# Kernel optimization log

Hardware: AMD Instinct MI355X
Metric: run time of the kernel (lower is better)

The kernel has to match this reference:

```python
import jax, jax.numpy as jnp
import numpy as np

NUM_CLASSES = 21
THRESH = 0.5
NEG_POS = 3
VAR0, VAR1 = 0.1, 0.2


def point_form(boxes):
    # center form (cx,cy,w,h) -> corner form (x1,y1,x2,y2)
    return jnp.concatenate([boxes[:, :2] - boxes[:, 2:] / 2,
                            boxes[:, :2] + boxes[:, 2:] / 2], axis=1)


def jaccard(a, b):
    # a: [N,4] corner form, b: [P,4] corner form -> IoU [N,P]
    lt = jnp.maximum(a[:, None, :2], b[None, :, :2])
    rb = jnp.minimum(a[:, None, 2:], b[None, :, 2:])
    wh = jnp.clip(rb - lt, 0.0)
    inter = wh[..., 0] * wh[..., 1]
    area_a = (a[:, 2] - a[:, 0]) * (a[:, 3] - a[:, 1])
    area_b = (b[:, 2] - b[:, 0]) * (b[:, 3] - b[:, 1])
    return inter / (area_a[:, None] + area_b[None, :] - inter)


def match_one(truths, labels, priors):
    # truths: [N,4] corner form, labels: [N] int, priors: [P,4] center form
    ov = jaccard(truths, point_form(priors))            # [N,P]
    best_prior_idx = jnp.argmax(ov, axis=1)             # [N] best prior per truth
    best_truth_ov = jnp.max(ov, axis=0)                 # [P]
    best_truth_idx = jnp.argmax(ov, axis=0)             # [P]
    # ensure each truth keeps its best prior
    best_truth_ov = best_truth_ov.at[best_prior_idx].set(2.0)
    best_truth_idx = best_truth_idx.at[best_prior_idx].set(
        jnp.arange(truths.shape[0], dtype=best_truth_idx.dtype))
    matches = truths[best_truth_idx]                    # [P,4]
    conf = labels[best_truth_idx] + 1                   # [P]
    conf = jnp.where(best_truth_ov < THRESH, 0, conf)
    # encode
    g_cxcy = ((matches[:, :2] + matches[:, 2:]) / 2 - priors[:, :2]) / (VAR0 * priors[:, 2:])
    g_wh = jnp.log((matches[:, 2:] - matches[:, :2]) / priors[:, 2:]) / VAR1
    return jnp.concatenate([g_cxcy, g_wh], axis=1), conf


def setup_inputs() -> dict:
    key = jax.random.key(0)
    k1, k2, k3, k4, k5, k6, k7 = jax.random.split(key, 7)
    B, P, C, N = 64, 24564, NUM_CLASSES, 16
    loc_data = jax.random.normal(k1, (B, P, 4), dtype=jnp.float32)
    conf_data = jax.random.normal(k2, (B, P, C), dtype=jnp.float32)
    # priors: valid center-form boxes
    ctr = 0.05 + 0.9 * jax.random.uniform(k3, (P, 2), dtype=jnp.float32)
    pwh = 0.05 + 0.25 * jax.random.uniform(k4, (P, 2), dtype=jnp.float32)
    priors = jnp.concatenate([ctr, pwh], axis=1)
    # truths: valid corner-form boxes
    xy1 = 0.7 * jax.random.uniform(k5, (B, N, 2), dtype=jnp.float32)
    twh = 0.05 + 0.2 * jax.random.uniform(k6, (B, N, 2), dtype=jnp.float32)
    truths = jnp.concatenate([xy1, xy1 + twh], axis=2)
    labels = jax.random.randint(k7, (B, N), 0, 20, dtype=jnp.int32)
    return {"loc_data": loc_data, "conf_data": conf_data, "priors": priors,
            "truths": truths, "labels": labels}


def reference(loc_data, conf_data, priors, truths, labels):
    B, P, C = conf_data.shape
    loc_t, conf_t = jax.vmap(lambda t, l: match_one(t, l, priors))(truths, labels)
    pos = conf_t > 0                                     # [B,P]

    # localization smooth-L1, summed over positives
    diff = loc_data - loc_t
    ad = jnp.abs(diff)
    sl1 = jnp.where(ad < 1.0, 0.5 * diff * diff, ad - 0.5)
    loss_l = jnp.sum(sl1 * pos[..., None].astype(loc_data.dtype))

    # per-prior CE = logsumexp - logit at matched class
    lse = jax.nn.logsumexp(conf_data, axis=2)            # [B,P]
    gathered = jnp.take_along_axis(conf_data, conf_t[..., None].astype(jnp.int32), axis=2)[..., 0]
    loss_c_all = lse - gathered

    # hard-negative mining via double argsort rank (pos zeroed first)
    loss_c_mine = jnp.where(pos, 0.0, loss_c_all)
    idx_rank = jnp.argsort(jnp.argsort(-loss_c_mine, axis=1), axis=1)
    num_pos = jnp.sum(pos, axis=1, keepdims=True)        # [B,1]
    num_neg = jnp.minimum(NEG_POS * num_pos, P - 1)
    neg = idx_rank < num_neg

    mask = pos | neg
    loss_c = jnp.sum(jnp.where(mask, loss_c_all, 0.0))

    n = jnp.sum(num_pos).astype(loc_data.dtype)
    return loss_l / n, loss_c / n
```

## Files before the change

### kernel.cpp

```cpp
#include <hip/hip_runtime.h>
#include <cstdint>
#include <cstddef>

#define B_ 64
#define P_ 24564
#define C_ 21
#define N_ 16
#define NPL_ 96
#define THRESH_ 0.5f


__device__ inline unsigned long long shfl_down_u64(unsigned long long v, int off) {
    unsigned lo = (unsigned)v, hi = (unsigned)(v >> 32);
    lo = __shfl_down(lo, off);
    hi = __shfl_down(hi, off);
    return ((unsigned long long)hi << 32) | lo;
}

__device__ inline void async_copy16(const float* g, float* l) {
    __builtin_amdgcn_global_load_lds(
        (const __attribute__((address_space(1))) void*)g,
        (__attribute__((address_space(3))) void*)l, 16, 0, 0);
}

__device__ inline float sl1_encode(float4 ld, float4 pr,
                                   float tx1, float ty1, float tx2, float ty2) {
    float gcx = ((tx1 + tx2) * 0.5f - pr.x) / (0.1f * pr.z);
    float gcy = ((ty1 + ty2) * 0.5f - pr.y) / (0.1f * pr.w);
    float gw  = __logf((tx2 - tx1) / pr.z) / 0.2f;
    float gh  = __logf((ty2 - ty1) / pr.w) / 0.2f;
    float g[4] = {gcx, gcy, gw, gh};
    float l[4] = {ld.x, ld.y, ld.z, ld.w};
    float s = 0.0f;
#pragma unroll
    for (int i = 0; i < 4; i++) {
        float d = l[i] - g[i];
        float ad = fabsf(d);
        s += (ad < 1.0f) ? 0.5f * d * d : ad - 0.5f;
    }
    return s;
}

__device__ inline void scan_hist(const int* h, int M, int kk,
                                 int* outB, int* outR) {
    int lane = threadIdx.x & 63;
    int CH = M >> 6;
    int base = M - (lane + 1) * CH;
    int s = 0;
    for (int j = 0; j < CH; j++) s += h[base + j];
    int incl = s;
#pragma unroll
    for (int off = 1; off < 64; off <<= 1) {
        int v = __shfl_up(incl, off);
        if (lane >= off) incl += v;
    }
    int excl = incl - s;
    if (excl < kk && excl + s >= kk) {
        int acc = excl;
        for (int bin = base + CH - 1; bin >= base; bin--) {
            int c = h[bin];
            if (acc + c >= kk) { *outB = bin; *outR = kk - acc; break; }
            acc += c;
        }
    }
}


__global__ __launch_bounds__(256) void
kF_fused(const float* __restrict__ loc,
         const float* __restrict__ conf,
         const float* __restrict__ priors,
         const float* __restrict__ truths,
         const int* __restrict__ labels,
         float* __restrict__ mine,
         float* __restrict__ part_ll,
         float* __restrict__ part_pce,
         int* __restrict__ part_np,
         unsigned long long* __restrict__ part_key) {
    int b = blockIdx.y, bx = blockIdx.x, t = threadIdx.x;
    int wid = t >> 6, lane = t & 63;
    __shared__ float scf[4 * 1536];
    __shared__ float sll[4], spc[4];
    __shared__ int snp[4];
    unsigned* skey = (unsigned*)scf;

    int base_p = bx * 256;
    int nvalid = min(256, P_ - base_p);
    int maxf4 = (nvalid * C_) >> 2;
    const float* gtile = conf + ((size_t)b * P_ + base_p) * C_;

    int p0 = base_p + t;
    bool valid = t < nvalid;
    float4 pr = ((const float4*)priors)[valid ? p0 : base_p];
    float px1 = pr.x - pr.z * 0.5f, py1 = pr.y - pr.w * 0.5f;
    float px2 = pr.x + pr.z * 0.5f, py2 = pr.y + pr.w * 0.5f;
    float ap = (px2 - px1) * (py2 - py1);

    float* slice = scf + wid * 1536;
    int wf4 = wid * 336;
#pragma unroll
    for (int i = 0; i < 6; i++) {
        int f4 = wf4 + i * 64 + lane;
        int s4 = (f4 < maxf4) ? f4 : (maxf4 - 1);
        async_copy16(gtile + (size_t)s4 * 4, slice + i * 256);
    }

    unsigned u[N_];
    float best = -1.0f;
    int bn = 0;
#pragma unroll
    for (int n = 0; n < N_; n++) {
        float4 tb = ((const float4*)truths)[b * N_ + n];
        float at = (tb.z - tb.x) * (tb.w - tb.y);
        float lx = fmaxf(tb.x, px1), ly = fmaxf(tb.y, py1);
        float rx = fminf(tb.z, px2), ry = fminf(tb.w, py2);
        float w = fmaxf(rx - lx, 0.0f), h = fmaxf(ry - ly, 0.0f);
        float inter = w * h;
        float iou = inter / (at + ap - inter);
        if (iou > best) { best = iou; bn = n; }
        u[n] = valid ? __float_as_uint(iou) : 0u;
    }
    int pos = (valid && best >= THRESH_) ? 1 : 0;
    int bl = labels[b * N_ + bn];

    asm volatile("s_waitcnt vmcnt(0)" ::: "memory");

    float ll = 0.0f, pce = 0.0f;
    int np = 0;
    if (valid) {
        int cls = pos ? (bl + 1) : 0;
        const float* row = scf + wid * 1536 + lane * 21;
        float ssum = 0.0f;
#pragma unroll
        for (int i = 0; i < 21; i++) ssum += __expf(row[i]);
        float g = row[cls];
        float lca = fmaxf(__logf(ssum) - g, 0.0f);

        mine[(size_t)b * P_ + p0] = pos ? 0.0f : lca;

        if (pos) {
            np = 1;
            pce = lca;
            float4 ld = ((const float4*)loc)[(size_t)b * P_ + p0];
            float4 tb = ((const float4*)truths)[b * N_ + bn];
            ll = sl1_encode(ld, pr, tb.x, tb.y, tb.z, tb.w);
        }
    }

    for (int off = 32; off; off >>= 1) {
        ll += __shfl_down(ll, off);
        pce += __shfl_down(pce, off);
        np += __shfl_down(np, off);
    }
    if (lane == 0) { sll[wid] = ll; spc[wid] = pce; snp[wid] = np; }

    __syncthreads();
#pragma unroll
    for (int n = 0; n < N_; n++) skey[n * 256 + t] = u[n];
    __syncthreads();

#pragma unroll
    for (int i = 0; i < 4; i++) {
        int n = wid + 4 * i;
        unsigned long long bk = 0ull;
#pragma unroll
        for (int q = 0; q < 4; q++) {
            int tt = lane + 64 * q;
            unsigned k32 = skey[n * 256 + tt];
            unsigned long long v = ((unsigned long long)k32 << 32) |
                                   (unsigned)~(unsigned)tt;
            bk = (v > bk) ? v : bk;
        }
        for (int off = 32; off; off >>= 1) {
            unsigned long long o = shfl_down_u64(bk, off);
            bk = (o > bk) ? o : bk;
        }
        if (lane == 0) {
            int twin = (int)~(unsigned)(bk & 0xFFFFFFFFull);
            int pwin = base_p + twin;
            part_key[(size_t)(b * NPL_ + bx) * N_ + n] =
                (bk & 0xFFFFFFFF00000000ull) | (unsigned)~(unsigned)pwin;
        }
    }
    if (t == 0) {
        float a = 0.0f, cc = 0.0f;
        int q = 0;
        for (int i = 0; i < 4; i++) { a += sll[i]; cc += spc[i]; q += snp[i]; }
        part_ll[b * NPL_ + bx] = a;
        part_pce[b * NPL_ + bx] = cc;
        part_np[b * NPL_ + bx] = q;
    }
}

__global__ __launch_bounds__(1024) void
kB_batch(const float* __restrict__ loc,
         const float* __restrict__ conf,
         const float* __restrict__ priors,
         const float* __restrict__ truths,
         const int* __restrict__ labels,
         const float* __restrict__ mine,
         const float* __restrict__ part_ll,
         const float* __restrict__ part_pce,
         const int* __restrict__ part_np,
         const unsigned long long* __restrict__ part_key,
         double* __restrict__ bll,
         double* __restrict__ bpc,
         int* __restrict__ bnp) {
    int b = blockIdx.x, t = threadIdx.x, wid = t >> 6, lane = t & 63;
    __shared__ float tr[N_ * 4];
    __shared__ int lb[N_];
    __shared__ unsigned long long skmax[N_];
    __shared__ int sp[N_];
    __shared__ float sdll, sdpce, sll_s, spc_s;
    __shared__ int sdnp, snp_s;
    __shared__ int hist[4 * 2048];
    __shared__ int hist2[1024];
    __shared__ int hist3[1024];
    __shared__ int sB[3], sR[3];
    __shared__ float wsum[16];
    __shared__ int wcgt[16];

    if (t < N_ * 4) tr[t] = truths[b * N_ * 4 + t];
    if (t < N_) { lb[t] = labels[b * N_ + t]; skmax[t] = 0ull; }
#pragma unroll
    for (int i = 0; i < 8; i++) hist[t + (i << 10)] = 0;
    hist2[t] = 0;
    hist3[t] = 0;
    if (t == 0) { sdll = 0.f; sdpce = 0.f; sdnp = 0; sll_s = 0.f; spc_s = 0.f; snp_s = 0; }
    __syncthreads();
    if (t < 256) {
        int n = t & 15, j = t >> 4;
        unsigned long long bk = 0ull;
        for (int i = j; i < NPL_; i += 16) {
            unsigned long long k = part_key[(size_t)(b * NPL_ + i) * N_ + n];
            bk = (k > bk) ? k : bk;
        }
        atomicMax(&skmax[n], bk);
    }
    if (t < 128) {
        float a = 0.f, c2 = 0.f;
        int q = 0;
        if (t < NPL_) {
            a = part_ll[b * NPL_ + t];
            c2 = part_pce[b * NPL_ + t];
            q = part_np[b * NPL_ + t];
        }
        for (int off = 32; off; off >>= 1) {
            a += __shfl_down(a, off);
            c2 += __shfl_down(c2, off);
            q += __shfl_down(q, off);
        }
        if (lane == 0) {
            atomicAdd(&sll_s, a);
            atomicAdd(&spc_s, c2);
            atomicAdd(&snp_s, q);
        }
    }
    __syncthreads();
    if (t < N_) sp[t] = (int)~(unsigned)(skmax[t] & 0xFFFFFFFFull);
    __syncthreads();
    if (t < N_) {
        int p = sp[t];
        bool last = true;
        for (int n = t + 1; n < N_; n++) if (sp[n] == p) last = false;
        if (last) {
            int nf = t;
            float4 pr = ((const float4*)priors)[p];
            float px1 = pr.x - pr.z * 0.5f, py1 = pr.y - pr.w * 0.5f;
            float px2 = pr.x + pr.z * 0.5f, py2 = pr.y + pr.w * 0.5f;
            float ap = (px2 - px1) * (py2 - py1);
            float best = -1.0f;
            int bti = 0;
            for (int n = 0; n < N_; n++) {
                float tx1 = tr[n * 4], ty1 = tr[n * 4 + 1];
                float tx2 = tr[n * 4 + 2], ty2 = tr[n * 4 + 3];
                float at = (tx2 - tx1) * (ty2 - ty1);
                float lx = fmaxf(tx1, px1), ly = fmaxf(ty1, py1);
                float rx = fminf(tx2, px2), ry = fminf(ty2, py2);
                float w = fmaxf(rx - lx, 0.0f), h = fmaxf(ry - ly, 0.0f);
                float inter = w * h;
                float iou = inter / (at + ap - inter);
                if (iou > best) { best = iou; bti = n; }
            }
            int pos_old = (best >= THRESH_) ? 1 : 0;
            const float* cp = conf + ((size_t)b * P_ + p) * C_;
            float ssum = 0.0f;
            for (int j = 0; j < C_; j++) ssum += __expf(cp[j]);
            float lse = __logf(ssum);
            float4 ld = ((const float4*)loc)[(size_t)b * P_ + p];
            float dll = sl1_encode(ld, pr, tr[nf * 4], tr[nf * 4 + 1],
                                   tr[nf * 4 + 2], tr[nf * 4 + 3]);
            float dpce = lse - cp[lb[nf] + 1];
            int dnp = 1 - pos_old;
            if (pos_old) {
                dll -= sl1_encode(ld, pr, tr[bti * 4], tr[bti * 4 + 1],
                                  tr[bti * 4 + 2], tr[bti * 4 + 3]);
                dpce -= lse - cp[lb[bti] + 1];
            }
            atomicAdd(&sdll, dll);
            atomicAdd(&sdpce, dpce);
            atomicAdd(&sdnp, dnp);
        }
    }

    unsigned omask = 0;
#pragma unroll
    for (int n = 0; n < N_; n++) {
        int p = sp[n];
        if ((p & 1023) == t) omask |= 1u << (p >> 10);
    }
    const float* v = mine + (size_t)b * P_;
    int nel = (t < (P_ - 23 * 1024)) ? 24 : 23;
    float xv[24];
#pragma unroll
    for (int i = 0; i < 24; i++) {
        float x = 0.0f;
        if (i < nel) x = v[t + (i << 10)];
        if ((omask >> i) & 1) x = 0.0f;
        xv[i] = x;
    }

    int rep = (wid & 3) << 11;
#pragma unroll
    for (int i = 0; i < 24; i++) {
        if (i < nel) {
            unsigned bb = __float_as_uint(xv[i]);
            atomicAdd(&hist[rep + (bb >> 20)], 1);
        }
    }
    __syncthreads();
    {
        int h0 = hist[t] + hist[t + 2048] + hist[t + 4096] + hist[t + 6144];
        int h1 = hist[t + 1024] + hist[t + 3072] + hist[t + 5120] + hist[t + 7168];
        hist[t] = h0;
        hist[t + 1024] = h1;
    }
    __syncthreads();

    int np = snp_s + sdnp;
    int k = np * 3;
    if (k > P_ - 1) k = P_ - 1;

    unsigned T = 0x7FFFFFFFu;
    if (k > 0) {
        if (wid == 0) scan_hist(hist, 2048, k, &sB[0], &sR[0]);
        __syncthreads();
        unsigned B1 = (unsigned)sB[0];
        int k1 = sR[0];
#pragma unroll
        for (int i = 0; i < 24; i++) {
            if (i < nel) {
                unsigned bb = __float_as_uint(xv[i]);
                if ((bb >> 20) == B1) atomicAdd(&hist2[(bb >> 10) & 0x3FF], 1);
            }
        }
        __syncthreads();
        if (wid == 0) scan_hist(hist2, 1024, k1, &sB[1], &sR[1]);
        __syncthreads();
        unsigned hi = (B1 << 10) | (unsigned)sB[1];
        int k2 = sR[1];
#pragma unroll
        for (int i = 0; i < 24; i++) {
            if (i < nel) {
                unsigned bb = __float_as_uint(xv[i]);
                if ((bb >> 10) == hi) atomicAdd(&hist3[bb & 0x3FF], 1);
            }
        }
        __syncthreads();
        if (wid == 0) scan_hist(hist3, 1024, k2, &sB[2], &sR[2]);
        __syncthreads();
        T = (hi << 10) | (unsigned)sB[2];
    }

    float psum = 0.0f;
    int cgt = 0;
#pragma unroll
    for (int i = 0; i < 24; i++) {
        if (__float_as_uint(xv[i]) > T) { psum += xv[i]; cgt++; }
    }
    for (int off = 32; off; off >>= 1) {
        psum += __shfl_down(psum, off);
        cgt += __shfl_down(cgt, off);
    }
    if (lane == 0) { wsum[wid] = psum; wcgt[wid] = cgt; }
    __syncthreads();
    if (t == 0) {
        float s2 = 0.0f;
        int cg = 0;
        for (int i = 0; i < 16; i++) { s2 += wsum[i]; cg += wcgt[i]; }
        int skrem = k - cg;
        double tot = (double)s2 + (double)skrem * (double)__uint_as_float(T);
        bll[b] = (double)(sll_s + sdll);
        bpc[b] = (double)(spc_s + sdpce) + tot;
        bnp[b] = np;
    }
}

__global__ void kC_final(const double* __restrict__ bll,
                         const double* __restrict__ bpc,
                         const int* __restrict__ bnp,
                         float* __restrict__ out) {
    int t = threadIdx.x;
    double a = bll[t], c = bpc[t];
    int n = bnp[t];
    for (int off = 32; off; off >>= 1) {
        a += __shfl_down(a, off);
        c += __shfl_down(c, off);
        n += __shfl_down(n, off);
    }
    if (t == 0) {
        double dn = (double)n;
        out[0] = (float)(a / dn);
        out[1] = (float)(c / dn);
    }
}


extern "C" void kernel_launch(void* const* d_in, const int* in_sizes, int n_in,
                              void* d_out, int out_size, void* d_ws, size_t ws_size,
                              hipStream_t stream) {
    const float* loc    = (const float*)d_in[0];
    const float* conf   = (const float*)d_in[1];
    const float* priors = (const float*)d_in[2];
    const float* truths = (const float*)d_in[3];
    const int*   labels = (const int*)d_in[4];
    float* out = (float*)d_out;

    char* ws = (char*)d_ws;
    unsigned long long* part_key = (unsigned long long*)(ws);
    float*  part_ll  = (float*)(ws + 786432);
    float*  part_pce = (float*)(ws + 811008);
    int*    part_np  = (int*)(ws + 835584);
    double* bll      = (double*)(ws + 860160);
    double* bpc      = (double*)(ws + 860672);
    int*    bnp      = (int*)(ws + 861184);
    float*  mine     = (float*)(ws + 1048576);

    hipLaunchKernelGGL(kF_fused, dim3(NPL_, B_), dim3(256), 0, stream,
                       loc, conf, priors, truths, labels,
                       mine, part_ll, part_pce, part_np, part_key);
    hipLaunchKernelGGL(kB_batch, dim3(B_), dim3(1024), 0, stream,
                       loc, conf, priors, truths, labels, mine,
                       part_ll, part_pce, part_np, part_key, bll, bpc, bnp);
    hipLaunchKernelGGL(kC_final, dim3(1), dim3(64), 0, stream, bll, bpc, bnp, out);
}
```

Measured before the change: 235.8 us.

## Split fused match kernel into separate logsumexp and matching kernels

```diff
diff --git a/kernel.cpp b/kernel.cpp
--- a/kernel.cpp
+++ b/kernel.cpp
@@ -67,11 +67,48 @@
 
 
 __global__ __launch_bounds__(256) void
-kF_fused(const float* __restrict__ loc,
+kS_lse(const float* __restrict__ conf,
+       float* __restrict__ mine,
+       float* __restrict__ lseA) {
+    int b = blockIdx.y, bx = blockIdx.x, t = threadIdx.x;
+    int wid = t >> 6, lane = t & 63;
+    __shared__ float scf[4 * 1536];
+
+    int base_p = bx * 256;
+    int nvalid = min(256, P_ - base_p);
+    int maxf4 = (nvalid * C_) >> 2;
+    const float* gtile = conf + ((size_t)b * P_ + base_p) * C_;
+
+    float* slice = scf + wid * 1536;
+    int wf4 = wid * 336;
+#pragma unroll
+    for (int i = 0; i < 6; i++) {
+        int f4 = wf4 + i * 64 + lane;
+        int s4 = (f4 < maxf4) ? f4 : (maxf4 - 1);
+        async_copy16(gtile + (size_t)s4 * 4, slice + i * 256);
+    }
+    asm volatile("s_waitcnt vmcnt(0)" ::: "memory");
+
+    if (t < nvalid) {
+        const float* row = slice + lane * 21;
+        float ssum = 0.0f;
+#pragma unroll
+        for (int i = 0; i < 21; i++) ssum += __expf(row[i]);
+        float lse = __logf(ssum);
+        float m0 = fmaxf(lse - row[0], 0.0f);
+        size_t gi = (size_t)b * P_ + base_p + t;
+        mine[gi] = m0;
+        lseA[gi] = lse;
+    }
+}
+
+__global__ __launch_bounds__(256) void
+kM_match(const float* __restrict__ loc,
          const float* __restrict__ conf,
          const float* __restrict__ priors,
          const float* __restrict__ truths,
          const int* __restrict__ labels,
+         const float* __restrict__ lseA,
          float* __restrict__ mine,
          float* __restrict__ part_ll,
          float* __restrict__ part_pce,
@@ -79,16 +116,12 @@
          unsigned long long* __restrict__ part_key) {
     int b = blockIdx.y, bx = blockIdx.x, t = threadIdx.x;
     int wid = t >> 6, lane = t & 63;
-    __shared__ float scf[4 * 1536];
+    __shared__ unsigned skey[N_ * 256];
     __shared__ float sll[4], spc[4];
     __shared__ int snp[4];
-    unsigned* skey = (unsigned*)scf;
 
     int base_p = bx * 256;
     int nvalid = min(256, P_ - base_p);
-    int maxf4 = (nvalid * C_) >> 2;
-    const float* gtile = conf + ((size_t)b * P_ + base_p) * C_;
-
     int p0 = base_p + t;
     bool valid = t < nvalid;
     float4 pr = ((const float4*)priors)[valid ? p0 : base_p];
@@ -96,16 +129,6 @@
     float px2 = pr.x + pr.z * 0.5f, py2 = pr.y + pr.w * 0.5f;
     float ap = (px2 - px1) * (py2 - py1);
 
-    float* slice = scf + wid * 1536;
-    int wf4 = wid * 336;
-#pragma unroll
-    for (int i = 0; i < 6; i++) {
-        int f4 = wf4 + i * 64 + lane;
-        int s4 = (f4 < maxf4) ? f4 : (maxf4 - 1);
-        async_copy16(gtile + (size_t)s4 * 4, slice + i * 256);
-    }
-
-    unsigned u[N_];
     float best = -1.0f;
     int bn = 0;
 #pragma unroll
@@ -118,33 +141,23 @@
         float inter = w * h;
         float iou = inter / (at + ap - inter);
         if (iou > best) { best = iou; bn = n; }
-        u[n] = valid ? __float_as_uint(iou) : 0u;
+        skey[n * 256 + t] = valid ? __float_as_uint(iou) : 0u;
     }
     int pos = (valid && best >= THRESH_) ? 1 : 0;
-    int bl = labels[b * N_ + bn];
-
-    asm volatile("s_waitcnt vmcnt(0)" ::: "memory");
 
     float ll = 0.0f, pce = 0.0f;
     int np = 0;
-    if (valid) {
-        int cls = pos ? (bl + 1) : 0;
-        const float* row = scf + wid * 1536 + lane * 21;
-        float ssum = 0.0f;
-#pragma unroll
-        for (int i = 0; i < 21; i++) ssum += __expf(row[i]);
-        float g = row[cls];
-        float lca = fmaxf(__logf(ssum) - g, 0.0f);
-
-        mine[(size_t)b * P_ + p0] = pos ? 0.0f : lca;
-
-        if (pos) {
-            np = 1;
-            pce = lca;
-            float4 ld = ((const float4*)loc)[(size_t)b * P_ + p0];
-            float4 tb = ((const float4*)truths)[b * N_ + bn];
-            ll = sl1_encode(ld, pr, tb.x, tb.y, tb.z, tb.w);
-        }
+    if (pos) {
+        int cls = labels[b * N_ + bn] + 1;
+        size_t gi = (size_t)b * P_ + p0;
+        float lse = lseA[gi];
+        float g = conf[gi * C_ + cls];
+        pce = fmaxf(lse - g, 0.0f);
+        mine[gi] = 0.0f;
+        float4 ld = ((const float4*)loc)[gi];
+        float4 tb = ((const float4*)truths)[b * N_ + bn];
+        ll = sl1_encode(ld, pr, tb.x, tb.y, tb.z, tb.w);
+        np = 1;
     }
 
     for (int off = 32; off; off >>= 1) {
@@ -154,9 +167,6 @@
     }
     if (lane == 0) { sll[wid] = ll; spc[wid] = pce; snp[wid] = np; }
 
-    __syncthreads();
-#pragma unroll
-    for (int n = 0; n < N_; n++) skey[n * 256 + t] = u[n];
     __syncthreads();
 
 #pragma unroll
@@ -435,9 +445,12 @@
     double* bpc      = (double*)(ws + 860672);
     int*    bnp      = (int*)(ws + 861184);
     float*  mine     = (float*)(ws + 1048576);
-
-    hipLaunchKernelGGL(kF_fused, dim3(NPL_, B_), dim3(256), 0, stream,
-                       loc, conf, priors, truths, labels,
+    float*  lseA     = (float*)(ws + 8388608);
+
+    hipLaunchKernelGGL(kS_lse, dim3(NPL_, B_), dim3(256), 0, stream,
+                       conf, mine, lseA);
+    hipLaunchKernelGGL(kM_match, dim3(NPL_, B_), dim3(256), 0, stream,
+                       loc, conf, priors, truths, labels, lseA,
                        mine, part_ll, part_pce, part_np, part_key);
     hipLaunchKernelGGL(kB_batch, dim3(B_), dim3(1024), 0, stream,
                        loc, conf, priors, truths, labels, mine,
```

New measurement: 253.1 us. 7.4% more time.
